# Optimization experiments

Hardware: AMD Instinct MI355X
Metric: run time of the kernel (lower is better)

Reference implementation:

```python
import jax, jax.numpy as jnp
import numpy as np

LN_EPS = 1e-5
L2_EPS = 1e-12
SCALE = 8.0

def setup_inputs() -> dict:
    key = jax.random.key(0)
    k0, k1, k2 = jax.random.split(key, 3)
    b, c, H, W = 16, 256, 64, 64
    heads, dim_head = 8, 32
    dim_inner = heads * dim_head  # 256
    x = jax.random.normal(k0, (b, c, H, W), dtype=jnp.float32)
    ln_gamma = jnp.ones((c,), jnp.float32)
    ln_beta = jnp.zeros((c,), jnp.float32)
    W_qkv = jax.random.normal(k1, (c, 3 * dim_inner), dtype=jnp.float32) * 0.02
    temperature = jnp.ones((heads,), jnp.float32)
    W_out = jax.random.normal(k2, (dim_inner, c), dtype=jnp.float32) * 0.02
    b_out = jnp.zeros((c,), jnp.float32)
    return {"x": x, "ln_gamma": ln_gamma, "ln_beta": ln_beta, "W_qkv": W_qkv,
            "temperature": temperature, "W_out": W_out, "b_out": b_out, "heads": heads}

def _l2norm(t):
    # F.normalize(t, dim=-1): divide by clamped L2 norm along last axis
    n = jnp.sqrt(jnp.sum(t * t, axis=-1, keepdims=True))
    return t / jnp.maximum(n, L2_EPS)

def reference(x, ln_gamma, ln_beta, W_qkv, temperature, W_out, b_out, heads):
    b, c, H, W = x.shape
    n = H * W
    dim_head = W_qkv.shape[1] // (3 * heads)
    # b c h w -> b (h w) c
    t = jnp.transpose(x, (0, 2, 3, 1)).reshape(b, n, c)
    # LayerNorm over channel dim (affine)
    mu = jnp.mean(t, axis=-1, keepdims=True)
    var = jnp.mean(jnp.square(t - mu), axis=-1, keepdims=True)
    t = (t - mu) * jax.lax.rsqrt(var + LN_EPS) * ln_gamma + ln_beta
    # qkv projection; split last dim as (qkv, heads, dim_head) -> (3, b, h, d, n)
    qkv = (t @ W_qkv).reshape(b, n, 3, heads, dim_head)
    qkv = jnp.transpose(qkv, (2, 0, 3, 4, 1))
    q, k, v = qkv[0], qkv[1], qkv[2]
    q = _l2norm(q) * jnp.exp(temperature)[None, :, None, None]
    k = _l2norm(k)
    # cross-covariance attention over channel dim: sim is [b, h, d, d]
    sim = jnp.einsum('bhin,bhjn->bhij', q, k) * SCALE
    attn = jax.nn.softmax(sim, axis=-1)
    out = jnp.einsum('bhij,bhjn->bhin', attn, v)  # [b, h, d, n]
    # b h d n -> b n (h d)
    out = jnp.transpose(out, (0, 3, 1, 2)).reshape(b, n, heads * dim_head)
    out = out @ W_out + b_out
    # b (h w) c -> b c h w
    return jnp.transpose(out.reshape(b, H, W, c), (0, 3, 1, 2))
```

## Files before the change

### kernel.cpp

```cpp
#include <hip/hip_runtime.h>

typedef unsigned short u16;
typedef __bf16 bf16x8 __attribute__((ext_vector_type(8)));
typedef float f32x4 __attribute__((ext_vector_type(4)));

#define MFMA(a, b, c) __builtin_amdgcn_mfma_f32_16x16x32_bf16((a), (b), (c), 0, 0, 0)

__device__ __forceinline__ u16 f2bf(float f) {
    unsigned u = __float_as_uint(f);
    unsigned r = (u + 0x7fffu + ((u >> 16) & 1u)) >> 16;
    return (u16)r;
}
__device__ __forceinline__ float bf2f(u16 h) { return __uint_as_float(((unsigned)h) << 16); }

typedef unsigned int u32_g __attribute__((address_space(1)));
typedef unsigned int u32_l __attribute__((address_space(3)));
__device__ __forceinline__ void gload16(const void* g, void* l) {
    __builtin_amdgcn_global_load_lds((const u32_g*)g, (u32_l*)l, 16, 0, 0);
}


__global__ __launch_bounds__(256) void k_ln(const float* __restrict__ x,
                                            const float* __restrict__ gamma,
                                            const float* __restrict__ beta,
                                            u16* __restrict__ xlnT, u16* __restrict__ xcn) {
    int bid = blockIdx.x;
    int b = bid >> 6, nt = bid & 63;
    int nb = nt * 64;
    __shared__ unsigned xsu[256 * 33];
    __shared__ float muv[64], rsv[64];
    __shared__ float redS[8 * 64], redS2[8 * 64];
    int t = threadIdx.x;
    {
        int np = t & 31;
        int c0 = t >> 5;
        const float* xp = x + ((size_t)b * 256) * 4096 + nb + np * 2;
        for (int i = 0; i < 32; i++) {
            int c = c0 + i * 8;
            float2 f = *(const float2*)(xp + (size_t)c * 4096);
            unsigned u = (unsigned)f2bf(f.x) | ((unsigned)f2bf(f.y) << 16);
            xsu[c * 33 + np] = u;
        }
    }
    __syncthreads();
    {
        int np = t & 31, q = t >> 5;
        float s0 = 0, s20 = 0, s1 = 0, s21 = 0;
        for (int i = 0; i < 32; i++) {
            unsigned u = xsu[(q * 32 + i) * 33 + np];
            float a = bf2f((u16)(u & 0xffffu));
            float bv = bf2f((u16)(u >> 16));
            s0 += a; s20 += a * a; s1 += bv; s21 += bv * bv;
        }
        redS[q * 64 + np * 2] = s0;  redS[q * 64 + np * 2 + 1] = s1;
        redS2[q * 64 + np * 2] = s20; redS2[q * 64 + np * 2 + 1] = s21;
    }
    __syncthreads();
    if (t < 64) {
        float s = 0, s2 = 0;
        for (int q = 0; q < 8; q++) { s += redS[q * 64 + t]; s2 += redS2[q * 64 + t]; }
        float m = s * (1.f / 256.f);
        float var = s2 * (1.f / 256.f) - m * m;
        muv[t] = m;
        rsv[t] = rsqrtf(var + 1e-5f);
    }
    __syncthreads();
    {
        int c4 = (t & 63) * 4;
        int ng = t >> 6;
        float g[4], e[4];
        for (int j = 0; j < 4; j++) { g[j] = gamma[c4 + j]; e[j] = beta[c4 + j]; }
        for (int i = 0; i < 16; i++) {
            int n = ng * 16 + i;
            float m = muv[n], rs = rsv[n];
            u16 h[4];
            for (int j = 0; j < 4; j++) {
                unsigned u = xsu[(c4 + j) * 33 + (n >> 1)];
                u16 raw = (n & 1) ? (u16)(u >> 16) : (u16)(u & 0xffffu);
                float v = (bf2f(raw) - m) * rs * g[j] + e[j];
                h[j] = f2bf(v);
            }
            uint2 w2;
            w2.x = (unsigned)h[0] | ((unsigned)h[1] << 16);
            w2.y = (unsigned)h[2] | ((unsigned)h[3] << 16);
            *(uint2*)(xlnT + ((size_t)(b * 4096 + nb + n)) * 256 + c4) = w2;
        }
    }
    {
        int lr = t & 7;
        int n0 = lr * 8;
        for (int it = 0; it < 8; it++) {
            int cg = (t >> 3) + it * 32;
            float g = gamma[cg], e = beta[cg];
            u16 hh[8];
            for (int jj = 0; jj < 8; jj++) {
                int nn = n0 + jj;
                unsigned u = xsu[cg * 33 + (nn >> 1)];
                u16 raw = (nn & 1) ? (u16)(u >> 16) : (u16)(u & 0xffffu);
                float v = (bf2f(raw) - muv[nn]) * rsv[nn] * g + e;
                hh[jj] = f2bf(v);
            }
            uint4 pk;
            pk.x = (unsigned)hh[0] | ((unsigned)hh[1] << 16);
            pk.y = (unsigned)hh[2] | ((unsigned)hh[3] << 16);
            pk.z = (unsigned)hh[4] | ((unsigned)hh[5] << 16);
            pk.w = (unsigned)hh[6] | ((unsigned)hh[7] << 16);
            *(uint4*)(xcn + ((size_t)(b * 256 + cg)) * 4096 + nb + n0) = pk;
        }
    }
}

__global__ __launch_bounds__(256) void k_prep(const float* __restrict__ Wqkv,
                                              const float* __restrict__ Wout,
                                              u16* __restrict__ WqkvT, u16* __restrict__ WvTn,
                                              u16* __restrict__ WoutT) {
    int i = blockIdx.x * 256 + threadIdx.x;
    if (i < 512 * 256) { int o = i >> 8, c = i & 255; WqkvT[i] = f2bf(Wqkv[c * 768 + o]); }
    if (i < 256 * 256) {
        int e = i >> 8, o = i & 255;
        WvTn[i] = f2bf(Wqkv[e * 768 + 512 + o]);
        WoutT[i] = f2bf(Wout[o * 256 + e]);
    }
}

__global__ __launch_bounds__(256) void k_gram(const u16* __restrict__ xcn, float* __restrict__ Gp) {
    int bid = blockIdx.x;
    int s = bid & 7, tile = (bid >> 3) & 3, b = bid >> 5;
    int tm = tile >> 1, tn = tile & 1;
    __shared__ __align__(16) u16 aT[128 * 32];
    __shared__ __align__(16) u16 bT[128 * 32];
    int t = threadIdx.x, w = t >> 6, lane = t & 63, l15 = lane & 15, quad = lane >> 4;
    int srow = lane >> 2;
    int g8 = (((lane & 3) ^ ((lane >> 3) & 3)) << 3);
    const u16* xb = xcn + (size_t)b * 256 * 4096 + (size_t)s * 512;
    const u16* gA = xb + (size_t)(tm * 128 + w * 32 + srow) * 4096 + g8;
    const u16* gB = xb + (size_t)(tn * 128 + w * 32 + srow) * 4096 + g8;
    u16* lA = aT + w * 1024;
    u16* lB = bT + w * 1024;
    int cOff = ((quad ^ ((l15 >> 1) & 3)) << 3);
    f32x4 acc[2][8];
    f32x4 z = {0.f, 0.f, 0.f, 0.f};
    for (int fm = 0; fm < 2; fm++)
        for (int fn = 0; fn < 8; fn++) acc[fm][fn] = z;
    for (int kt = 0; kt < 16; kt++) {
        int kb = kt * 32;
        if (kt) __syncthreads();
        gload16(gA + kb, lA);
        gload16(gA + 16 * 4096 + kb, lA + 512);
        gload16(gB + kb, lB);
        gload16(gB + 16 * 4096 + kb, lB + 512);
        __syncthreads();
        bf16x8 af0 = *(const bf16x8*)&aT[(w * 32 + l15) * 32 + cOff];
        bf16x8 af1 = *(const bf16x8*)&aT[(w * 32 + 16 + l15) * 32 + cOff];
        for (int fn = 0; fn < 8; fn++) {
            bf16x8 bfr = *(const bf16x8*)&bT[(fn * 16 + l15) * 32 + cOff];
            acc[0][fn] = MFMA(af0, bfr, acc[0][fn]);
            acc[1][fn] = MFMA(af1, bfr, acc[1][fn]);
        }
    }
    float* gp = Gp + (size_t)(s * 16 + b) * 65536;
    for (int fm = 0; fm < 2; fm++)
        for (int fn = 0; fn < 8; fn++)
            for (int r = 0; r < 4; r++) {
                int row = tm * 128 + w * 32 + fm * 16 + quad * 4 + r;
                int col = tn * 128 + fn * 16 + l15;
                gp[row * 256 + col] = acc[fm][fn][r];
            }
}

__global__ __launch_bounds__(256) void k_g2b(const float* __restrict__ Gp,
                                             u16* __restrict__ Ghi, u16* __restrict__ Glo) {
    int idx = blockIdx.x * 256 + threadIdx.x;
    const float4* p = (const float4*)Gp + idx;
    float4 s = p[0];
#pragma unroll
    for (int j = 1; j < 8; j++) {
        float4 v = p[(size_t)j * 262144];
        s.x += v.x; s.y += v.y; s.z += v.z; s.w += v.w;
    }
    u16 h0 = f2bf(s.x), h1 = f2bf(s.y), h2 = f2bf(s.z), h3 = f2bf(s.w);
    u16 l0 = f2bf(s.x - bf2f(h0)), l1 = f2bf(s.y - bf2f(h1));
    u16 l2 = f2bf(s.z - bf2f(h2)), l3 = f2bf(s.w - bf2f(h3));
    uint2 ph; ph.x = (unsigned)h0 | ((unsigned)h1 << 16); ph.y = (unsigned)h2 | ((unsigned)h3 << 16);
    uint2 pl; pl.x = (unsigned)l0 | ((unsigned)l1 << 16); pl.y = (unsigned)l2 | ((unsigned)l3 << 16);
    *(uint2*)(Ghi + (size_t)idx * 4) = ph;
    *(uint2*)(Glo + (size_t)idx * 4) = pl;
}

__global__ __launch_bounds__(256) void k_sq(const u16* __restrict__ A,
                                            const u16* __restrict__ Ghi, const u16* __restrict__ Glo,
                                            u16* __restrict__ Shi, u16* __restrict__ Slo) {
    __shared__ __align__(16) u16 aT[128 * 32];
    __shared__ __align__(16) u16 bT[128 * 32];
    int bid = blockIdx.x;
    int b = bid >> 3;
    int r2 = bid & 7;
    int mbase = (r2 >> 1) * 128, nbase = (r2 & 1) * 128;
    int t = threadIdx.x, w = t >> 6, lane = t & 63, l15 = lane & 15, quad = lane >> 4;
    int srow = lane >> 2;
    int g8 = (((lane & 3) ^ ((lane >> 3) & 3)) << 3);
    const u16* gA = A + (size_t)(mbase + w * 32 + srow) * 256 + g8;
    const u16* gBh = Ghi + (size_t)b * 65536 + (size_t)(nbase + w * 32 + srow) * 256 + g8;
    const u16* gBl = Glo + (size_t)b * 65536 + (size_t)(nbase + w * 32 + srow) * 256 + g8;
    u16* lA = aT + w * 1024;
    u16* lB = bT + w * 1024;
    int cOff = ((quad ^ ((l15 >> 1) & 3)) << 3);
    f32x4 acc[2][8];
    f32x4 z = {0.f, 0.f, 0.f, 0.f};
    for (int fm = 0; fm < 2; fm++)
        for (int fn = 0; fn < 8; fn++) acc[fm][fn] = z;
    for (int kt = 0; kt < 16; kt++) {
        int kb = (kt & 7) * 32;
        const u16* gB = (kt < 8) ? gBh : gBl;
        if (kt) __syncthreads();
        gload16(gA + kb, lA);
        gload16(gA + 16 * 256 + kb, lA + 512);
        gload16(gB + kb, lB);
        gload16(gB + 16 * 256 + kb, lB + 512);
        __syncthreads();
        bf16x8 af0 = *(const bf16x8*)&aT[(w * 32 + l15) * 32 + cOff];
        bf16x8 af1 = *(const bf16x8*)&aT[(w * 32 + 16 + l15) * 32 + cOff];
        for (int fn = 0; fn < 8; fn++) {
            bf16x8 bfr = *(const bf16x8*)&bT[(fn * 16 + l15) * 32 + cOff];
            acc[0][fn] = MFMA(af0, bfr, acc[0][fn]);
            acc[1][fn] = MFMA(af1, bfr, acc[1][fn]);
        }
    }
    for (int fm = 0; fm < 2; fm++)
        for (int fn = 0; fn < 8; fn++)
            for (int r = 0; r < 4; r++) {
                int row = mbase + w * 32 + fm * 16 + quad * 4 + r;
                int col = nbase + fn * 16 + l15;
                float v = acc[fm][fn][r];
                u16 hi = f2bf(v);
                Shi[((size_t)b * 512 + row) * 256 + col] = hi;
                Slo[((size_t)b * 512 + row) * 256 + col] = f2bf(v - bf2f(hi));
            }
}

__global__ __launch_bounds__(256) void k_gemm(const u16* __restrict__ A, size_t aStrB,
                                              const u16* __restrict__ Bb, size_t bStrB,
                                              int mtiles, int ntiles,
                                              u16* __restrict__ o16, float* __restrict__ o32,
                                              const float* __restrict__ bias,
                                              size_t oStrB, int oRstr, int mode) {
    __shared__ __align__(16) u16 aT[128 * 32];
    __shared__ __align__(16) u16 bT[128 * 32];
    int bid = blockIdx.x;
    int per_b = mtiles * ntiles;
    int b = bid / per_b;
    int r2 = bid % per_b;
    int mbase = (r2 / ntiles) * 128, nbase = (r2 % ntiles) * 128;
    int t = threadIdx.x, w = t >> 6, lane = t & 63, l15 = lane & 15, quad = lane >> 4;
    const u16* Ap = A + (size_t)b * aStrB;
    const u16* Bp = Bb + (size_t)b * bStrB;
    int srow = lane >> 2;
    int g8 = (((lane & 3) ^ ((lane >> 3) & 3)) << 3);
    const u16* gA = Ap + (size_t)(mbase + w * 32 + srow) * 256 + g8;
    const u16* gB = Bp + (size_t)(nbase + w * 32 + srow) * 256 + g8;
    u16* lA = aT + w * 1024;
    u16* lB = bT + w * 1024;
    int cOff = ((quad ^ ((l15 >> 1) & 3)) << 3);
    f32x4 acc[2][8];
    f32x4 z = {0.f, 0.f, 0.f, 0.f};
    for (int fm = 0; fm < 2; fm++)
        for (int fn = 0; fn < 8; fn++) acc[fm][fn] = z;
    for (int kt = 0; kt < 8; kt++) {
        int kb = kt * 32;
        if (kt) __syncthreads();
        gload16(gA + kb, lA);
        gload16(gA + 16 * 256 + kb, lA + 512);
        gload16(gB + kb, lB);
        gload16(gB + 16 * 256 + kb, lB + 512);
        __syncthreads();
        bf16x8 af0 = *(const bf16x8*)&aT[(w * 32 + l15) * 32 + cOff];
        bf16x8 af1 = *(const bf16x8*)&aT[(w * 32 + 16 + l15) * 32 + cOff];
        for (int fn = 0; fn < 8; fn++) {
            bf16x8 bfr = *(const bf16x8*)&bT[(fn * 16 + l15) * 32 + cOff];
            acc[0][fn] = MFMA(af0, bfr, acc[0][fn]);
            acc[1][fn] = MFMA(af1, bfr, acc[1][fn]);
        }
    }
    if (mode == 0) {
        for (int fm = 0; fm < 2; fm++)
            for (int fn = 0; fn < 8; fn++)
                for (int r = 0; r < 4; r++) {
                    int row = mbase + w * 32 + fm * 16 + quad * 4 + r;
                    int col = nbase + fn * 16 + l15;
                    o16[(size_t)b * oStrB + (size_t)row * oRstr + col] = f2bf(acc[fm][fn][r]);
                }
    } else {
        for (int fm = 0; fm < 2; fm++)
            for (int fn = 0; fn < 8; fn++)
                for (int r = 0; r < 4; r++) {
                    int row = mbase + w * 32 + fm * 16 + quad * 4 + r;
                    int col = nbase + fn * 16 + l15;
                    o32[(size_t)b * oStrB + (size_t)row * oRstr + col] = acc[fm][fn][r] + bias[row];
                }
    }
}

__global__ __launch_bounds__(256) void k_attn(const u16* __restrict__ Shi,
                                              const u16* __restrict__ Slo,
                                              const u16* __restrict__ WqkvT,
                                              const u16* __restrict__ WoutT,
                                              const float* __restrict__ temp,
                                              u16* __restrict__ M_all) {
    int bh = blockIdx.x;
    int b = bh >> 3, h = bh & 7;
    __shared__ u16 sqh[32 * 264], sql[32 * 264], skh[32 * 264], wq[32 * 264], wk[32 * 264];
    __shared__ u16 wo[256 * 40];
    __shared__ u16 attnT[32 * 40];
    __shared__ float simS[32 * 33];
    __shared__ float redn[4 * 64];
    __shared__ float scq[32], sck[32];
    int t = threadIdx.x, w = t >> 6, lane = t & 63, l15 = lane & 15, quad = lane >> 4;
    {
        int r = t >> 3, cc0 = (t & 7) * 32;
        const u16* gqh = Shi + ((size_t)(b * 512) + h * 32 + r) * 256 + cc0;
        const u16* gql = Slo + ((size_t)(b * 512) + h * 32 + r) * 256 + cc0;
        const u16* gkh = Shi + ((size_t)(b * 512) + 256 + h * 32 + r) * 256 + cc0;
        const u16* gwq = WqkvT + (size_t)(h * 32 + r) * 256 + cc0;
        const u16* gwk = WqkvT + (size_t)(256 + h * 32 + r) * 256 + cc0;
#pragma unroll
        for (int k = 0; k < 4; k++) {
            *(uint4*)&sqh[r * 264 + cc0 + k * 8] = *(const uint4*)(gqh + k * 8);
            *(uint4*)&sql[r * 264 + cc0 + k * 8] = *(const uint4*)(gql + k * 8);
            *(uint4*)&skh[r * 264 + cc0 + k * 8] = *(const uint4*)(gkh + k * 8);
            *(uint4*)&wq[r * 264 + cc0 + k * 8] = *(const uint4*)(gwq + k * 8);
            *(uint4*)&wk[r * 264 + cc0 + k * 8] = *(const uint4*)(gwk + k * 8);
        }
        const u16* gwo = WoutT + (size_t)t * 256 + h * 32;
#pragma unroll
        for (int k = 0; k < 4; k++) *(uint4*)&wo[t * 40 + k * 8] = *(const uint4*)(gwo + k * 8);
    }
    __syncthreads();
    {
        int rn = t & 63, cc = t >> 6;
        int e0 = cc * 64;
        float s = 0.f;
        if (rn < 32) {
            const u16* ph = &sqh[rn * 264];
            const u16* pl = &sql[rn * 264];
            const u16* pb = &wq[rn * 264];
            for (int e = 0; e < 64; e++)
                s += (bf2f(ph[e0 + e]) + bf2f(pl[e0 + e])) * bf2f(pb[e0 + e]);
        } else {
            const u16* ph = &skh[(rn - 32) * 264];
            const u16* pb = &wk[(rn - 32) * 264];
            for (int e = 0; e < 64; e++)
                s += bf2f(ph[e0 + e]) * bf2f(pb[e0 + e]);
        }
        redn[cc * 64 + rn] = s;
    }
    {
        int iq = w >> 1, jq = w & 1;
        f32x4 acc = {0.f, 0.f, 0.f, 0.f};
        for (int s8 = 0; s8 < 8; s8++) {
            bf16x8 a = *(const bf16x8*)&sqh[(iq * 16 + l15) * 264 + s8 * 32 + quad * 8];
            bf16x8 bb = *(const bf16x8*)&wk[(jq * 16 + l15) * 264 + s8 * 32 + quad * 8];
            acc = MFMA(a, bb, acc);
        }
        for (int s8 = 0; s8 < 8; s8++) {
            bf16x8 a = *(const bf16x8*)&sql[(iq * 16 + l15) * 264 + s8 * 32 + quad * 8];
            bf16x8 bb = *(const bf16x8*)&wk[(jq * 16 + l15) * 264 + s8 * 32 + quad * 8];
            acc = MFMA(a, bb, acc);
        }
        for (int r = 0; r < 4; r++)
            simS[(iq * 16 + quad * 4 + r) * 33 + jq * 16 + l15] = acc[r];
    }
    __syncthreads();
    if (t < 32)
        scq[t] = expf(temp[h]) * 8.0f /
                 fmaxf(sqrtf(redn[t] + redn[64 + t] + redn[128 + t] + redn[192 + t]), 1e-12f);
    else if (t < 64) {
        int d = t - 32;
        sck[d] = 1.0f / fmaxf(sqrtf(redn[32 + d] + redn[96 + d] + redn[160 + d] + redn[224 + d]), 1e-12f);
    }
    __syncthreads();
    if (t < 32) {
        float row[32];
        float m = -1e30f, sqv = scq[t];
#pragma unroll
        for (int j = 0; j < 32; j++) {
            float v = simS[t * 33 + j] * sqv * sck[j];
            row[j] = v; m = fmaxf(m, v);
        }
        float s = 0.f;
#pragma unroll
        for (int j = 0; j < 32; j++) { float p = expf(row[j] - m); row[j] = p; s += p; }
        float inv = 1.f / s;
#pragma unroll
        for (int j = 0; j < 32; j++) attnT[j * 40 + t] = f2bf(row[j] * inv);
    }
    __syncthreads();
    {
        f32x4 z = {0.f, 0.f, 0.f, 0.f};
        for (int mf = 0; mf < 4; mf++) {
            bf16x8 a = *(const bf16x8*)&wo[((w * 4 + mf) * 16 + l15) * 40 + quad * 8];
            for (int nf = 0; nf < 2; nf++) {
                bf16x8 bb = *(const bf16x8*)&attnT[(nf * 16 + l15) * 40 + quad * 8];
                f32x4 d = MFMA(a, bb, z);
                for (int r = 0; r < 4; r++) {
                    int c = (w * 4 + mf) * 16 + quad * 4 + r;
                    M_all[((size_t)(b * 256) + c) * 256 + h * 32 + nf * 16 + l15] = f2bf(d[r]);
                }
            }
        }
    }
}

extern "C" void kernel_launch(void* const* d_in, const int* in_sizes, int n_in,
                              void* d_out, int out_size, void* d_ws, size_t ws_size,
                              hipStream_t stream) {
    const float* x     = (const float*)d_in[0];
    const float* gamma = (const float*)d_in[1];
    const float* beta  = (const float*)d_in[2];
    const float* Wqkv  = (const float*)d_in[3];
    const float* temp  = (const float*)d_in[4];
    const float* Wout  = (const float*)d_in[5];
    const float* bout  = (const float*)d_in[6];
    float* out = (float*)d_out;

    char* ws = (char*)d_ws;
    size_t off = 0;
    auto alloc = [&](size_t nbytes) -> void* {
        void* p = ws + off;
        off = (off + nbytes + 255) & ~(size_t)255;
        return p;
    };
    u16* xlnT   = (u16*)alloc((size_t)16 * 4096 * 256 * 2);
    u16* xcn    = (u16*)alloc((size_t)16 * 256 * 4096 * 2);
    u16* WqkvT  = (u16*)alloc((size_t)512 * 256 * 2);
    u16* WvTn   = (u16*)alloc((size_t)256 * 256 * 2);
    u16* WoutT  = (u16*)alloc((size_t)256 * 256 * 2);
    float* Gp   = (float*)alloc((size_t)8 * 16 * 65536 * 4);
    u16* Gbh    = (u16*)alloc((size_t)16 * 65536 * 2);
    u16* Gbl    = (u16*)alloc((size_t)16 * 65536 * 2);
    u16* Sqh    = (u16*)alloc((size_t)16 * 512 * 256 * 2);
    u16* Sql    = (u16*)alloc((size_t)16 * 512 * 256 * 2);
    u16* M_all  = (u16*)alloc((size_t)16 * 256 * 256 * 2);
    u16* F      = (u16*)alloc((size_t)16 * 256 * 256 * 2);
    (void)ws_size; (void)in_sizes; (void)n_in; (void)out_size;

    hipLaunchKernelGGL(k_ln, dim3(1024), dim3(256), 0, stream, x, gamma, beta, xlnT, xcn);
    hipLaunchKernelGGL(k_prep, dim3(768), dim3(256), 0, stream, Wqkv, Wout, WqkvT, WvTn, WoutT);
    hipLaunchKernelGGL(k_gram, dim3(512), dim3(256), 0, stream, xcn, Gp);
    hipLaunchKernelGGL(k_g2b, dim3(1024), dim3(256), 0, stream, Gp, Gbh, Gbl);
    hipLaunchKernelGGL(k_sq, dim3(128), dim3(256), 0, stream, WqkvT, Gbh, Gbl, Sqh, Sql);
    hipLaunchKernelGGL(k_attn, dim3(128), dim3(256), 0, stream, Sqh, Sql, WqkvT, WoutT, temp, M_all);
    hipLaunchKernelGGL(k_gemm, dim3(64), dim3(256), 0, stream,
                       M_all, (size_t)65536, WvTn, (size_t)0, 2, 2,
                       F, (float*)nullptr, (const float*)nullptr,
                       (size_t)65536, 256, 0);
    hipLaunchKernelGGL(k_gemm, dim3(1024), dim3(256), 0, stream,
                       F, (size_t)65536, xlnT, (size_t)4096 * 256, 2, 32,
                       (u16*)nullptr, out, bout,
                       (size_t)256 * 4096, 4096, 1);
}
```

Baseline: 218.7 us.

## Restructure LayerNorm kernel to keep inputs in registers with smaller tiles

The LayerNorm kernel now handles 32 positions per block instead of 64, doubling the grid. Each thread keeps its 16 channels by 2 positions of fp32 input in registers and computes partial statistics directly. That removes the bf16 staging of raw x in shared memory and the second pass over LDS. Normalized values go straight to the row-major output with 16-byte stores, and a small padded LDS tile handles the channel-major transposed output. Statistics are now computed from fp32 rather than bf16-rounded inputs, which changes numerics slightly, and the smaller tiles shorten the contiguous global reads per channel row.

```diff
diff --git a/kernel.cpp b/kernel.cpp
--- a/kernel.cpp
+++ b/kernel.cpp
@@ -25,88 +25,88 @@
                                             const float* __restrict__ beta,
                                             u16* __restrict__ xlnT, u16* __restrict__ xcn) {
     int bid = blockIdx.x;
-    int b = bid >> 6, nt = bid & 63;
-    int nb = nt * 64;
-    __shared__ unsigned xsu[256 * 33];
-    __shared__ float muv[64], rsv[64];
-    __shared__ float redS[8 * 64], redS2[8 * 64];
+    int b = bid >> 7, nt = bid & 127;
+    int nb = nt * 32;
+    __shared__ float redS[32 * 17], redS2[32 * 17];
+    __shared__ float muv[32], rsv[32];
+    __shared__ float gs[256], es[256];
+    __shared__ unsigned xst[256 * 17];
     int t = threadIdx.x;
-    {
-        int np = t & 31;
-        int c0 = t >> 5;
-        const float* xp = x + ((size_t)b * 256) * 4096 + nb + np * 2;
-        for (int i = 0; i < 32; i++) {
-            int c = c0 + i * 8;
-            float2 f = *(const float2*)(xp + (size_t)c * 4096);
-            unsigned u = (unsigned)f2bf(f.x) | ((unsigned)f2bf(f.y) << 16);
-            xsu[c * 33 + np] = u;
-        }
-    }
-    __syncthreads();
-    {
-        int np = t & 31, q = t >> 5;
-        float s0 = 0, s20 = 0, s1 = 0, s21 = 0;
-        for (int i = 0; i < 32; i++) {
-            unsigned u = xsu[(q * 32 + i) * 33 + np];
-            float a = bf2f((u16)(u & 0xffffu));
-            float bv = bf2f((u16)(u >> 16));
-            s0 += a; s20 += a * a; s1 += bv; s21 += bv * bv;
-        }
-        redS[q * 64 + np * 2] = s0;  redS[q * 64 + np * 2 + 1] = s1;
-        redS2[q * 64 + np * 2] = s20; redS2[q * 64 + np * 2 + 1] = s21;
-    }
-    __syncthreads();
-    if (t < 64) {
-        float s = 0, s2 = 0;
-        for (int q = 0; q < 8; q++) { s += redS[q * 64 + t]; s2 += redS2[q * 64 + t]; }
+    int np = t & 15, cg = t >> 4;
+    gs[t] = gamma[t];
+    es[t] = beta[t];
+    const float* xp = x + ((size_t)(b * 256 + cg * 16)) * 4096 + nb + np * 2;
+    float2 v[16];
+    float s0 = 0.f, s1 = 0.f, s20 = 0.f, s21 = 0.f;
+#pragma unroll
+    for (int i = 0; i < 16; i++) {
+        float2 f = *(const float2*)(xp + (size_t)i * 4096);
+        v[i] = f;
+        s0 += f.x; s20 += f.x * f.x;
+        s1 += f.y; s21 += f.y * f.y;
+    }
+    redS[(2 * np) * 17 + cg] = s0;
+    redS[(2 * np + 1) * 17 + cg] = s1;
+    redS2[(2 * np) * 17 + cg] = s20;
+    redS2[(2 * np + 1) * 17 + cg] = s21;
+    __syncthreads();
+    if (t < 32) {
+        float s = 0.f, s2 = 0.f;
+#pragma unroll
+        for (int g = 0; g < 16; g++) { s += redS[t * 17 + g]; s2 += redS2[t * 17 + g]; }
         float m = s * (1.f / 256.f);
         float var = s2 * (1.f / 256.f) - m * m;
         muv[t] = m;
         rsv[t] = rsqrtf(var + 1e-5f);
     }
     __syncthreads();
+    float m0 = muv[2 * np], r0 = rsv[2 * np];
+    float m1 = muv[2 * np + 1], r1 = rsv[2 * np + 1];
+    u16 hA[16], hB[16];
+#pragma unroll
+    for (int i = 0; i < 16; i++) {
+        float g = gs[cg * 16 + i], e = es[cg * 16 + i];
+        float a = (v[i].x - m0) * r0 * g + e;
+        float c2 = (v[i].y - m1) * r1 * g + e;
+        u16 ha = f2bf(a), hb = f2bf(c2);
+        hA[i] = ha; hB[i] = hb;
+        xst[(cg * 16 + i) * 17 + np] = (unsigned)ha | ((unsigned)hb << 16);
+    }
     {
-        int c4 = (t & 63) * 4;
-        int ng = t >> 6;
-        float g[4], e[4];
-        for (int j = 0; j < 4; j++) { g[j] = gamma[c4 + j]; e[j] = beta[c4 + j]; }
-        for (int i = 0; i < 16; i++) {
-            int n = ng * 16 + i;
-            float m = muv[n], rs = rsv[n];
-            u16 h[4];
-            for (int j = 0; j < 4; j++) {
-                unsigned u = xsu[(c4 + j) * 33 + (n >> 1)];
-                u16 raw = (n & 1) ? (u16)(u >> 16) : (u16)(u & 0xffffu);
-                float v = (bf2f(raw) - m) * rs * g[j] + e[j];
-                h[j] = f2bf(v);
-            }
-            uint2 w2;
-            w2.x = (unsigned)h[0] | ((unsigned)h[1] << 16);
-            w2.y = (unsigned)h[2] | ((unsigned)h[3] << 16);
-            *(uint2*)(xlnT + ((size_t)(b * 4096 + nb + n)) * 256 + c4) = w2;
-        }
-    }
-    {
-        int lr = t & 7;
-        int n0 = lr * 8;
-        for (int it = 0; it < 8; it++) {
-            int cg = (t >> 3) + it * 32;
-            float g = gamma[cg], e = beta[cg];
-            u16 hh[8];
-            for (int jj = 0; jj < 8; jj++) {
-                int nn = n0 + jj;
-                unsigned u = xsu[cg * 33 + (nn >> 1)];
-                u16 raw = (nn & 1) ? (u16)(u >> 16) : (u16)(u & 0xffffu);
-                float v = (bf2f(raw) - muv[nn]) * rsv[nn] * g + e;
-                hh[jj] = f2bf(v);
-            }
-            uint4 pk;
-            pk.x = (unsigned)hh[0] | ((unsigned)hh[1] << 16);
-            pk.y = (unsigned)hh[2] | ((unsigned)hh[3] << 16);
-            pk.z = (unsigned)hh[4] | ((unsigned)hh[5] << 16);
-            pk.w = (unsigned)hh[6] | ((unsigned)hh[7] << 16);
-            *(uint4*)(xcn + ((size_t)(b * 256 + cg)) * 4096 + nb + n0) = pk;
-        }
+        u16* dst0 = xlnT + ((size_t)(b * 4096 + nb + 2 * np)) * 256 + cg * 16;
+        uint4 qa, qb;
+        qa.x = (unsigned)hA[0] | ((unsigned)hA[1] << 16);
+        qa.y = (unsigned)hA[2] | ((unsigned)hA[3] << 16);
+        qa.z = (unsigned)hA[4] | ((unsigned)hA[5] << 16);
+        qa.w = (unsigned)hA[6] | ((unsigned)hA[7] << 16);
+        qb.x = (unsigned)hA[8] | ((unsigned)hA[9] << 16);
+        qb.y = (unsigned)hA[10] | ((unsigned)hA[11] << 16);
+        qb.z = (unsigned)hA[12] | ((unsigned)hA[13] << 16);
+        qb.w = (unsigned)hA[14] | ((unsigned)hA[15] << 16);
+        *(uint4*)dst0 = qa;
+        *(uint4*)(dst0 + 8) = qb;
+        u16* dst1 = dst0 + 256;
+        qa.x = (unsigned)hB[0] | ((unsigned)hB[1] << 16);
+        qa.y = (unsigned)hB[2] | ((unsigned)hB[3] << 16);
+        qa.z = (unsigned)hB[4] | ((unsigned)hB[5] << 16);
+        qa.w = (unsigned)hB[6] | ((unsigned)hB[7] << 16);
+        qb.x = (unsigned)hB[8] | ((unsigned)hB[9] << 16);
+        qb.y = (unsigned)hB[10] | ((unsigned)hB[11] << 16);
+        qb.z = (unsigned)hB[12] | ((unsigned)hB[13] << 16);
+        qb.w = (unsigned)hB[14] | ((unsigned)hB[15] << 16);
+        *(uint4*)dst1 = qa;
+        *(uint4*)(dst1 + 8) = qb;
+    }
+    __syncthreads();
+#pragma unroll
+    for (int j = 0; j < 4; j++) {
+        int row = (t >> 2) + j * 64, part = t & 3;
+        uint4 q;
+        q.x = xst[row * 17 + part * 4 + 0];
+        q.y = xst[row * 17 + part * 4 + 1];
+        q.z = xst[row * 17 + part * 4 + 2];
+        q.w = xst[row * 17 + part * 4 + 3];
+        *(uint4*)(xcn + ((size_t)(b * 256 + row)) * 4096 + nb + part * 8) = q;
     }
 }
 
@@ -443,7 +443,7 @@
     u16* F      = (u16*)alloc((size_t)16 * 256 * 256 * 2);
     (void)ws_size; (void)in_sizes; (void)n_in; (void)out_size;
 
-    hipLaunchKernelGGL(k_ln, dim3(1024), dim3(256), 0, stream, x, gamma, beta, xlnT, xcn);
+    hipLaunchKernelGGL(k_ln, dim3(2048), dim3(256), 0, stream, x, gamma, beta, xlnT, xcn);
     hipLaunchKernelGGL(k_prep, dim3(768), dim3(256), 0, stream, Wqkv, Wout, WqkvT, WvTn, WoutT);
     hipLaunchKernelGGL(k_gram, dim3(512), dim3(256), 0, stream, xcn, Gp);
     hipLaunchKernelGGL(k_g2b, dim3(1024), dim3(256), 0, stream, Gp, Gbh, Gbl);
```

New measurement: 224.3 us. 1.03x slower.
